# Kernel tuning notes

Hardware: AMD Instinct MI355X
Metric: run time of the kernel (lower is better)

The kernel has to match this reference:

```python
import jax, jax.numpy as jnp
from jax import lax
import numpy as np

B, P, M1, M2, M3 = 128, 168, 2, 2, 2
M = M1 * M2 * M3
HIDC, HIDR, HIDS, CK, SKIP, HW = 50, 50, 5, 6, 24, 24
PT = (P - CK) // SKIP  # int((P-Ck)/skip) = 6
L = P - CK + 1         # 163


def gru(xs, w_ih, w_hh, b_ih, b_hh, hid):
    # xs: [T, N, in]; torch nn.GRU cell semantics, h0 = 0. Returns final h: [N, hid].
    def step(h, x):
        gi = x @ w_ih.T + b_ih
        gh = h @ w_hh.T + b_hh
        ir, iz, inn = jnp.split(gi, 3, axis=-1)
        hr, hz, hn = jnp.split(gh, 3, axis=-1)
        r = jax.nn.sigmoid(ir + hr)
        z = jax.nn.sigmoid(iz + hz)
        n = jnp.tanh(inn + r * hn)
        return (1.0 - z) * n + z * h, None
    h0 = jnp.zeros((xs.shape[1], hid), xs.dtype)
    h, _ = lax.scan(step, h0, xs)
    return h


def setup_inputs() -> dict:
    key = jax.random.key(0)
    ks = jax.random.split(key, 16)
    O = P * HIDC * CK  # 50400 conv output channels
    d = {
        'x': jax.random.normal(ks[0], (B, P, M1, M2, M3), jnp.float32),
        'conv_w': jax.random.normal(ks[1], (O, P, M1, M2, M3), jnp.float32) * 0.02,
        'conv_b': jax.random.normal(ks[2], (O,), jnp.float32) * 0.02,
        'g1_wih': jax.random.normal(ks[3], (3 * HIDR, HIDC), jnp.float32) * 0.1,
        'g1_whh': jax.random.normal(ks[4], (3 * HIDR, HIDR), jnp.float32) * 0.1,
        'g1_bih': jax.random.normal(ks[5], (3 * HIDR,), jnp.float32) * 0.1,
        'g1_bhh': jax.random.normal(ks[6], (3 * HIDR,), jnp.float32) * 0.1,
        'gs_wih': jax.random.normal(ks[7], (3 * HIDS, HIDC), jnp.float32) * 0.1,
        'gs_whh': jax.random.normal(ks[8], (3 * HIDS, HIDS), jnp.float32) * 0.1,
        'gs_bih': jax.random.normal(ks[9], (3 * HIDS,), jnp.float32) * 0.1,
        'gs_bhh': jax.random.normal(ks[10], (3 * HIDS,), jnp.float32) * 0.1,
        'l1_w': jax.random.normal(ks[11], (M, HIDR + SKIP * HIDS), jnp.float32) * 0.1,
        'l1_b': jax.random.normal(ks[12], (M,), jnp.float32) * 0.1,
        'hw_w': jax.random.normal(ks[13], (1, HW), jnp.float32) * 0.1,
        'hw_b': jax.random.normal(ks[14], (1,), jnp.float32) * 0.1,
    }
    return d


def reference(x, conv_w, conv_b, g1_wih, g1_whh, g1_bih, g1_bhh,
              gs_wih, gs_whh, gs_bih, gs_bhh, l1_w, l1_b, hw_w, hw_b):
    # Conv3d with kernel == full spatial extent is a dense matmul over (P*m1*m2*m3).
    xf = x.reshape(B, -1)                       # [B, P*M]
    wf = conv_w.reshape(conv_w.shape[0], -1)    # [O, P*M]
    c = jax.nn.relu(xf @ wf.T + conv_b)         # [B, O]
    c = c.reshape(B, HIDC, CK, P)
    # Diagonal strided sum (the torch triple loop): res1[b,c,t] = sum_k c[b,c,k,k+t]
    res1 = sum(c[:, :, k, k:k + L] for k in range(CK))  # [B, HIDC, L]
    # dropout: eval mode (identity)
    r = gru(jnp.transpose(res1, (2, 0, 1)), g1_wih, g1_whh, g1_bih, g1_bhh, HIDR)  # [B, HIDR]
    # skip GRU
    s = res1[:, :, -PT * SKIP:]                          # [B, HIDC, PT*SKIP]
    s = s.reshape(B, HIDC, PT, SKIP)
    s = jnp.transpose(s, (2, 0, 3, 1)).reshape(PT, B * SKIP, HIDC)
    hs = gru(s, gs_wih, gs_whh, gs_bih, gs_bhh, HIDS)    # [B*SKIP, HIDS]
    hs = hs.reshape(B, SKIP * HIDS)
    r = jnp.concatenate([r, hs], axis=1)                 # [B, HIDR + SKIP*HIDS]
    res = r @ l1_w.T + l1_b                              # [B, M]
    # highway (AR) component over the last HW timesteps
    z = x[:, -HW:].reshape(B, HW, M)                     # [B, HW, M]
    z = jnp.transpose(z, (0, 2, 1)).reshape(-1, HW)      # [B*M, HW]
    z = z @ hw_w.T + hw_b                                # [B*M, 1]
    res = res + z.reshape(B, M)
    res = jax.nn.sigmoid(res)
    return res.reshape(B, M1, M2, M3)
```

## Files before the change

kernel.cpp:

```cpp
#include <hip/hip_runtime.h>
#include <hip/hip_bf16.h>
#include <cstdint>


typedef __attribute__((ext_vector_type(8))) short short8;
typedef __attribute__((ext_vector_type(4))) float f32x4;
typedef __attribute__((ext_vector_type(2))) float f32x2;

__device__ __forceinline__ unsigned short bf16rn(float f) {
    unsigned u = __float_as_uint(f);
    return (unsigned short)((u + 0x7FFFu + ((u >> 16) & 1u)) >> 16);
}
__device__ __forceinline__ unsigned pk2(float a, float b) {
    return ((unsigned)bf16rn(b) << 16) | (unsigned)bf16rn(a);
}
__device__ __forceinline__ uint4 pack8(float4 f0, float4 f1) {
    uint4 u;
    u.x = pk2(f0.x, f0.y); u.y = pk2(f0.z, f0.w);
    u.z = pk2(f1.x, f1.y); u.w = pk2(f1.z, f1.w);
    return u;
}
__device__ __forceinline__ float bf2f(unsigned short u) {
    return __uint_as_float((unsigned)u << 16);
}
__device__ __forceinline__ float sigmf(float x) {
    return __builtin_amdgcn_rcpf(1.f + __expf(-x));
}
__device__ __forceinline__ float tanhf_(float x) {
    return 1.f - 2.f * __builtin_amdgcn_rcpf(__expf(2.f * x) + 1.f);
}

__global__ __launch_bounds__(256, 2)
void k1_conv_gemm(const float* __restrict__ x, const float* __restrict__ w,
                  const float* __restrict__ bias, unsigned short* __restrict__ c) {
    __shared__ uint4 a_lds[8 * 129];
    __shared__ uint4 b_lds[8 * 113];
    const int tid  = threadIdx.x;
    const int n0   = blockIdx.x * 112;
    const int wave = tid >> 6, lane = tid & 63;
    const int quad = lane >> 4, m16 = lane & 15;

    f32x4 acc[2][7];
#pragma unroll
    for (int i = 0; i < 2; ++i)
#pragma unroll
        for (int j = 0; j < 7; ++j) acc[i][j] = (f32x4){0.f, 0.f, 0.f, 0.f};

    float4 pa[4][2];
    float4 pb[4][2];

    auto issue = [&](int kb) {
#pragma unroll
        for (int i = 0; i < 4; ++i) {
            int row = (tid >> 3) + 32 * i;
            const float* gp = x + row * 1344 + kb + (tid & 7) * 8;
            pa[i][0] = *reinterpret_cast<const float4*>(gp);
            pa[i][1] = *reinterpret_cast<const float4*>(gp + 4);
        }
#pragma unroll
        for (int i = 0; i < 4; ++i) {
            int idx = tid + 256 * i;
            if (idx < 896) {
                int row = idx >> 3;
                const float* gp = w + (size_t)(n0 + row) * 1344 + kb + (idx & 7) * 8;
                pb[i][0] = *reinterpret_cast<const float4*>(gp);
                pb[i][1] = *reinterpret_cast<const float4*>(gp + 4);
            }
        }
    };

    issue(0);
    for (int kb = 0; kb < 1344; kb += 64) {
#pragma unroll
        for (int i = 0; i < 4; ++i) {
            int idx = tid + 256 * i;
            int row = idx >> 3, ks = idx & 7;
            a_lds[ks * 129 + row] = pack8(pa[i][0], pa[i][1]);
        }
#pragma unroll
        for (int i = 0; i < 4; ++i) {
            int idx = tid + 256 * i;
            if (idx < 896) {
                int row = idx >> 3, ks = idx & 7;
                b_lds[ks * 113 + row] = pack8(pb[i][0], pb[i][1]);
            }
        }
        __syncthreads();
        if (kb + 64 < 1344) issue(kb + 64);
#pragma unroll
        for (int half = 0; half < 2; ++half) {
            const int kp = half * 4 + quad;
            short8 af[2], bfr[7];
#pragma unroll
            for (int rt = 0; rt < 2; ++rt)
                af[rt] = ((const short8*)a_lds)[kp * 129 + wave * 32 + rt * 16 + m16];
#pragma unroll
            for (int ct = 0; ct < 7; ++ct)
                bfr[ct] = ((const short8*)b_lds)[kp * 113 + ct * 16 + m16];
#pragma unroll
            for (int rt = 0; rt < 2; ++rt)
#pragma unroll
                for (int ct = 0; ct < 7; ++ct)
                    acc[rt][ct] = __builtin_amdgcn_mfma_f32_16x16x32_bf16(
                        af[rt], bfr[ct], acc[rt][ct], 0, 0, 0);
        }
        __syncthreads();
    }
#pragma unroll
    for (int ct = 0; ct < 7; ++ct) {
        int col = n0 + ct * 16 + m16;
        float bv = bias[col];
#pragma unroll
        for (int rt = 0; rt < 2; ++rt) {
#pragma unroll
            for (int r = 0; r < 4; ++r) {
                int grow = wave * 32 + rt * 16 + quad * 4 + r;
                float v = acc[rt][ct][r] + bv;
                v = fmaxf(v, 0.f);
                c[(size_t)grow * 50400 + col] = bf16rn(v);
            }
        }
    }
}

__attribute__((amdgpu_waves_per_eu(1, 1)))
__global__ __launch_bounds__(256, 1)
void k_fused2(const unsigned short* __restrict__ c,
              const float* __restrict__ g1_wih, const float* __restrict__ g1_whh,
              const float* __restrict__ g1_bih, const float* __restrict__ g1_bhh,
              const float* __restrict__ gs_wih, const float* __restrict__ gs_whh,
              const float* __restrict__ gs_bih, const float* __restrict__ gs_bhh,
              const float* __restrict__ l1_w, const float* __restrict__ l1_b,
              const float* __restrict__ x, const float* __restrict__ hw_w,
              const float* __restrict__ hw_b, float* __restrict__ out) {
    __shared__ float rloc[50 * 164];
    __shared__ float gi1l[163 * 150];
    __shared__ float gi2l[144 * 15];
    __shared__ __align__(16) float hl[64];
    __shared__ float r1l[50];
    __shared__ float hsl[120];

    const int b    = blockIdx.x;
    const int tid  = threadIdx.x;
    const int wave = tid >> 6, lane = tid & 63;

    const unsigned short* cb = c + (size_t)b * 50400;
    for (int idx = tid; idx < 8150; idx += 256) {
        int hc = idx / 163, t = idx - hc * 163;
        int base = hc * 1008 + t;
        float s = 0.f;
#pragma unroll
        for (int k = 0; k < 6; ++k) s += bf2f(cb[base + 169 * k]);
        rloc[hc * 164 + t] = s;
    }
    __syncthreads();

    for (int task = wave; task < 6; task += 4) {
        const int tB   = (task >> 1) * 64 + lane;
        const int half = task & 1;
        if (tB < 163) {
            float xcol[50];
#pragma unroll
            for (int j = 0; j < 50; ++j) xcol[j] = rloc[j * 164 + tB];

            const int c0 = __builtin_amdgcn_readfirstlane(half * 75);
            const float* wbase = g1_wih + c0 * 50;
            float* gdst = &gi1l[tB * 150 + c0];
            for (int cc = 0; cc < 75; ++cc) {
                const float* wp = wbase + cc * 50;
                float acc = g1_bih[c0 + cc];
#pragma unroll
                for (int j = 0; j < 50; ++j) acc += xcol[j] * wp[j];
                gdst[cc] = acc;
            }
            if (tB >= 19) {
                const int r2 = tB - 19;
                const int d0 = __builtin_amdgcn_readfirstlane(half * 8);
                const int ncol = half ? 7 : 8;
                float* g2 = &gi2l[r2 * 15];
                for (int cc = 0; cc < ncol; ++cc) {
                    const float* wp = gs_wih + (d0 + cc) * 50;
                    float acc = gs_bih[d0 + cc];
#pragma unroll
                    for (int j = 0; j < 50; ++j) acc += xcol[j] * wp[j];
                    g2[d0 + cc] = acc;
                }
            }
        }
    }
    __syncthreads();
    if (wave != 0) return;

    const int lc = (lane < 50) ? lane : 49;
    f32x2 wr2[25], wz2[25], wn2[25];
    {
        const float* wrp = g1_whh + lc * 50;
        const float* wzp = g1_whh + (50 + lc) * 50;
        const float* wnp = g1_whh + (100 + lc) * 50;
#pragma unroll
        for (int j = 0; j < 25; ++j) {
            wr2[j] = *reinterpret_cast<const f32x2*>(wrp + 2 * j);
            wz2[j] = *reinterpret_cast<const f32x2*>(wzp + 2 * j);
            wn2[j] = *reinterpret_cast<const f32x2*>(wnp + 2 * j);
        }
#pragma unroll
        for (int j = 0; j < 25; ++j) {
            asm volatile("" : "+v"(wr2[j]));
            asm volatile("" : "+v"(wz2[j]));
            asm volatile("" : "+v"(wn2[j]));
        }
    }
    const float bhr = g1_bhh[lc], bhz = g1_bhh[50 + lc], bhn = g1_bhh[100 + lc];
    hl[lane] = 0.f;
    float hcur = 0.f;

    float gir = gi1l[lc] + bhr, giz = gi1l[50 + lc] + bhz, gin = gi1l[100 + lc];
    int off = 150;
    for (int t = 0; t < 163; ++t) {
        float ngir = 0.f, ngiz = 0.f, ngin = 0.f;
        if (t < 162) {
            ngir = gi1l[off + lc] + bhr;
            ngiz = gi1l[off + 50 + lc] + bhz;
            ngin = gi1l[off + 100 + lc];
        }
        float4 h4[12];
#pragma unroll
        for (int j4 = 0; j4 < 12; ++j4)
            h4[j4] = *reinterpret_cast<const float4*>(&hl[4 * j4]);
        f32x2 ht; ht.x = hl[48]; ht.y = hl[49];
        f32x2 ar = {0.f, 0.f}, az = {0.f, 0.f}, an = {0.f, 0.f};
#pragma unroll
        for (int j4 = 0; j4 < 12; ++j4) {
            f32x2 h0; h0.x = h4[j4].x; h0.y = h4[j4].y;
            f32x2 h1; h1.x = h4[j4].z; h1.y = h4[j4].w;
            ar += wr2[2 * j4] * h0; ar += wr2[2 * j4 + 1] * h1;
            az += wz2[2 * j4] * h0; az += wz2[2 * j4 + 1] * h1;
            an += wn2[2 * j4] * h0; an += wn2[2 * j4 + 1] * h1;
        }
        ar += wr2[24] * ht; az += wz2[24] * ht; an += wn2[24] * ht;
        float rg = sigmf(gir + ar.x + ar.y);
        float zg = sigmf(giz + az.x + az.y);
        float ng = tanhf_(gin + rg * (bhn + an.x + an.y));
        hcur = fmaf(zg, hcur - ng, ng);
        hl[lane] = hcur;
        gir = ngir; giz = ngiz; gin = ngin;
        off += 150;
    }
    if (lane < 50) r1l[lane] = hcur;

    if (lane < 24) {
        float h2[5] = {0.f, 0.f, 0.f, 0.f, 0.f};
        for (int pt = 0; pt < 6; ++pt) {
            const float* g2 = &gi2l[(pt * 24 + lane) * 15];
            float gi[15];
#pragma unroll
            for (int i = 0; i < 15; ++i) gi[i] = g2[i];
            float gh[15];
#pragma unroll
            for (int i = 0; i < 15; ++i) {
                float s = gs_bhh[i];
#pragma unroll
                for (int j = 0; j < 5; ++j) s += gs_whh[i * 5 + j] * h2[j];
                gh[i] = s;
            }
#pragma unroll
            for (int u = 0; u < 5; ++u) {
                float rg = sigmf(gi[u] + gh[u]);
                float zg = sigmf(gi[5 + u] + gh[5 + u]);
                float ng = tanhf_(gi[10 + u] + rg * gh[10 + u]);
                h2[u] = (1.f - zg) * ng + zg * h2[u];
            }
        }
#pragma unroll
        for (int u = 0; u < 5; ++u) hsl[lane * 5 + u] = h2[u];
    }

    if (lane < 8) {
        const int m = lane;
        float acc = l1_b[m];
        const float* wrow = l1_w + m * 170;
#pragma unroll
        for (int j = 0; j < 50; ++j) acc += r1l[j] * wrow[j];
#pragma unroll
        for (int j = 0; j < 120; ++j) acc += hsl[j] * wrow[50 + j];
        float z = hw_b[0];
        const float* xb = x + (size_t)b * 1344 + 144 * 8 + m;
#pragma unroll
        for (int wi = 0; wi < 24; ++wi) z += xb[wi * 8] * hw_w[wi];
        out[b * 8 + m] = __builtin_amdgcn_rcpf(1.f + __expf(-(acc + z)));
    }
}

extern "C" void kernel_launch(void* const* d_in, const int* in_sizes, int n_in,
                              void* d_out, int out_size, void* d_ws, size_t ws_size,
                              hipStream_t stream) {
    const float* x      = (const float*)d_in[0];
    const float* conv_w = (const float*)d_in[1];
    const float* conv_b = (const float*)d_in[2];
    const float* g1_wih = (const float*)d_in[3];
    const float* g1_whh = (const float*)d_in[4];
    const float* g1_bih = (const float*)d_in[5];
    const float* g1_bhh = (const float*)d_in[6];
    const float* gs_wih = (const float*)d_in[7];
    const float* gs_whh = (const float*)d_in[8];
    const float* gs_bih = (const float*)d_in[9];
    const float* gs_bhh = (const float*)d_in[10];
    const float* l1_w   = (const float*)d_in[11];
    const float* l1_b   = (const float*)d_in[12];
    const float* hw_w   = (const float*)d_in[13];
    const float* hw_b   = (const float*)d_in[14];
    float* out = (float*)d_out;

    unsigned short* c = (unsigned short*)d_ws;

    hipLaunchKernelGGL(k1_conv_gemm, dim3(450), dim3(256), 0, stream, x, conv_w, conv_b, c);
    hipLaunchKernelGGL(k_fused2,     dim3(128), dim3(256), 0, stream,
                       c, g1_wih, g1_whh, g1_bih, g1_bhh,
                       gs_wih, gs_whh, gs_bih, gs_bhh,
                       l1_w, l1_b, x, hw_w, hw_b, out);
}
```

Baseline: 531.9 us.

## Fuse diagonal strided sum into conv GEMM epilogue and widen GRU kernel to 384 threads

New measurement: 522.5 us. No clear change (-1.8%).

```diff
diff --git a/kernel.cpp b/kernel.cpp
--- a/kernel.cpp
+++ b/kernel.cpp
@@ -20,9 +20,6 @@
     u.z = pk2(f1.x, f1.y); u.w = pk2(f1.z, f1.w);
     return u;
 }
-__device__ __forceinline__ float bf2f(unsigned short u) {
-    return __uint_as_float((unsigned)u << 16);
-}
 __device__ __forceinline__ float sigmf(float x) {
     return __builtin_amdgcn_rcpf(1.f + __expf(-x));
 }
@@ -32,22 +29,24 @@
 
 __global__ __launch_bounds__(256, 2)
 void k1_conv_gemm(const float* __restrict__ x, const float* __restrict__ w,
-                  const float* __restrict__ bias, unsigned short* __restrict__ c) {
+                  const float* __restrict__ bias, float* __restrict__ res1) {
     __shared__ uint4 a_lds[8 * 129];
-    __shared__ uint4 b_lds[8 * 113];
+    __shared__ uint4 b_lds[8 * 97];
     const int tid  = threadIdx.x;
-    const int n0   = blockIdx.x * 112;
+    const int hc   = blockIdx.x / 11;
+    const int tt   = blockIdx.x - hc * 11;
+    const int t0   = tt * 16;
     const int wave = tid >> 6, lane = tid & 63;
     const int quad = lane >> 4, m16 = lane & 15;
 
-    f32x4 acc[2][7];
+    f32x4 acc[2][6];
 #pragma unroll
     for (int i = 0; i < 2; ++i)
 #pragma unroll
-        for (int j = 0; j < 7; ++j) acc[i][j] = (f32x4){0.f, 0.f, 0.f, 0.f};
+        for (int j = 0; j < 6; ++j) acc[i][j] = (f32x4){0.f, 0.f, 0.f, 0.f};
 
     float4 pa[4][2];
-    float4 pb[4][2];
+    float4 pb[3][2];
 
     auto issue = [&](int kb) {
 #pragma unroll
@@ -58,14 +57,16 @@
             pa[i][1] = *reinterpret_cast<const float4*>(gp + 4);
         }
 #pragma unroll
-        for (int i = 0; i < 4; ++i) {
+        for (int i = 0; i < 3; ++i) {
             int idx = tid + 256 * i;
-            if (idx < 896) {
-                int row = idx >> 3;
-                const float* gp = w + (size_t)(n0 + row) * 1344 + kb + (idx & 7) * 8;
-                pb[i][0] = *reinterpret_cast<const float4*>(gp);
-                pb[i][1] = *reinterpret_cast<const float4*>(gp + 4);
-            }
+            int rn  = idx >> 3;
+            int k   = rn >> 4, ti = rn & 15;
+            int t   = t0 + ti;
+            int tc  = (t < 163) ? t : t0;
+            const float* gp = w + (size_t)(hc * 1008 + k * 169 + tc) * 1344
+                                + kb + (idx & 7) * 8;
+            pb[i][0] = *reinterpret_cast<const float4*>(gp);
+            pb[i][1] = *reinterpret_cast<const float4*>(gp + 4);
         }
     };
 
@@ -78,54 +79,54 @@
             a_lds[ks * 129 + row] = pack8(pa[i][0], pa[i][1]);
         }
 #pragma unroll
-        for (int i = 0; i < 4; ++i) {
+        for (int i = 0; i < 3; ++i) {
             int idx = tid + 256 * i;
-            if (idx < 896) {
-                int row = idx >> 3, ks = idx & 7;
-                b_lds[ks * 113 + row] = pack8(pb[i][0], pb[i][1]);
-            }
+            int row = idx >> 3, ks = idx & 7;
+            b_lds[ks * 97 + row] = pack8(pb[i][0], pb[i][1]);
         }
         __syncthreads();
         if (kb + 64 < 1344) issue(kb + 64);
 #pragma unroll
         for (int half = 0; half < 2; ++half) {
             const int kp = half * 4 + quad;
-            short8 af[2], bfr[7];
+            short8 af[2], bfr[6];
 #pragma unroll
             for (int rt = 0; rt < 2; ++rt)
                 af[rt] = ((const short8*)a_lds)[kp * 129 + wave * 32 + rt * 16 + m16];
 #pragma unroll
-            for (int ct = 0; ct < 7; ++ct)
-                bfr[ct] = ((const short8*)b_lds)[kp * 113 + ct * 16 + m16];
+            for (int ct = 0; ct < 6; ++ct)
+                bfr[ct] = ((const short8*)b_lds)[kp * 97 + ct * 16 + m16];
 #pragma unroll
             for (int rt = 0; rt < 2; ++rt)
 #pragma unroll
-                for (int ct = 0; ct < 7; ++ct)
+                for (int ct = 0; ct < 6; ++ct)
                     acc[rt][ct] = __builtin_amdgcn_mfma_f32_16x16x32_bf16(
                         af[rt], bfr[ct], acc[rt][ct], 0, 0, 0);
         }
         __syncthreads();
     }
-#pragma unroll
-    for (int ct = 0; ct < 7; ++ct) {
-        int col = n0 + ct * 16 + m16;
-        float bv = bias[col];
+    const int t = t0 + m16;
+    if (t < 163) {
+        float bv[6];
+#pragma unroll
+        for (int ct = 0; ct < 6; ++ct) bv[ct] = bias[hc * 1008 + ct * 169 + t];
 #pragma unroll
         for (int rt = 0; rt < 2; ++rt) {
 #pragma unroll
             for (int r = 0; r < 4; ++r) {
                 int grow = wave * 32 + rt * 16 + quad * 4 + r;
-                float v = acc[rt][ct][r] + bv;
-                v = fmaxf(v, 0.f);
-                c[(size_t)grow * 50400 + col] = bf16rn(v);
-            }
-        }
-    }
-}
-
-__attribute__((amdgpu_waves_per_eu(1, 1)))
-__global__ __launch_bounds__(256, 1)
-void k_fused2(const unsigned short* __restrict__ c,
+                float s = 0.f;
+#pragma unroll
+                for (int ct = 0; ct < 6; ++ct)
+                    s += fmaxf(acc[rt][ct][r] + bv[ct], 0.f);
+                res1[(size_t)grow * 8150 + hc * 163 + t] = s;
+            }
+        }
+    }
+}
+
+__global__ __launch_bounds__(384, 1)
+void k_fused3(const float* __restrict__ res1g,
               const float* __restrict__ g1_wih, const float* __restrict__ g1_whh,
               const float* __restrict__ g1_bih, const float* __restrict__ g1_bhh,
               const float* __restrict__ gs_wih, const float* __restrict__ gs_whh,
@@ -136,6 +137,7 @@
     __shared__ float rloc[50 * 164];
     __shared__ float gi1l[163 * 150];
     __shared__ float gi2l[144 * 15];
+    __shared__ float l1wl[8 * 170];
     __shared__ __align__(16) float hl[64];
     __shared__ float r1l[50];
     __shared__ float hsl[120];
@@ -144,20 +146,19 @@
     const int tid  = threadIdx.x;
     const int wave = tid >> 6, lane = tid & 63;
 
-    const unsigned short* cb = c + (size_t)b * 50400;
-    for (int idx = tid; idx < 8150; idx += 256) {
-        int hc = idx / 163, t = idx - hc * 163;
-        int base = hc * 1008 + t;
-        float s = 0.f;
-#pragma unroll
-        for (int k = 0; k < 6; ++k) s += bf2f(cb[base + 169 * k]);
-        rloc[hc * 164 + t] = s;
+    {
+        const float* src = res1g + (size_t)b * 8150;
+        for (int idx = tid; idx < 8150; idx += 384) {
+            int hc = idx / 163, t = idx - hc * 163;
+            rloc[hc * 164 + t] = src[idx];
+        }
+        for (int idx = tid; idx < 1360; idx += 384) l1wl[idx] = l1_w[idx];
     }
     __syncthreads();
 
-    for (int task = wave; task < 6; task += 4) {
-        const int tB   = (task >> 1) * 64 + lane;
-        const int half = task & 1;
+    {
+        const int tB   = (wave >> 1) * 64 + lane;
+        const int half = wave & 1;
         if (tB < 163) {
             float xcol[50];
 #pragma unroll
@@ -278,7 +279,7 @@
     if (lane < 8) {
         const int m = lane;
         float acc = l1_b[m];
-        const float* wrow = l1_w + m * 170;
+        const float* wrow = &l1wl[m * 170];
 #pragma unroll
         for (int j = 0; j < 50; ++j) acc += r1l[j] * wrow[j];
 #pragma unroll
@@ -311,11 +312,12 @@
     const float* hw_b   = (const float*)d_in[14];
     float* out = (float*)d_out;
 
-    unsigned short* c = (unsigned short*)d_ws;
-
-    hipLaunchKernelGGL(k1_conv_gemm, dim3(450), dim3(256), 0, stream, x, conv_w, conv_b, c);
-    hipLaunchKernelGGL(k_fused2,     dim3(128), dim3(256), 0, stream,
-                       c, g1_wih, g1_whh, g1_bih, g1_bhh,
+    float* res1g = (float*)d_ws;
+
+    hipLaunchKernelGGL(k1_conv_gemm, dim3(550), dim3(256), 0, stream,
+                       x, conv_w, conv_b, res1g);
+    hipLaunchKernelGGL(k_fused3,     dim3(128), dim3(384), 0, stream,
+                       res1g, g1_wih, g1_whh, g1_bih, g1_bhh,
                        gs_wih, gs_whh, gs_bih, gs_bhh,
                        l1_w, l1_b, x, hw_w, hw_b, out);
 }
```
